# Performance work log

Hardware: AMD Instinct MI355X
Metric: run time of the kernel (lower is better)

The kernel has to match this reference:

```python
import jax, jax.numpy as jnp
import numpy as np

D_MODEL = 1024
HEADS = 16
D_K = D_MODEL // HEADS
B, S = 2, 2048
NEG = -1e9


def setup_inputs() -> dict:
    key = jax.random.key(0)
    ks = jax.random.split(key, 12)
    sc = 1.0 / np.sqrt(D_MODEL)
    inp = {
        'query': jax.random.normal(ks[0], (B, S, D_MODEL), jnp.float32),
        'key': jax.random.normal(ks[1], (B, S, D_MODEL), jnp.float32),
        'value': jax.random.normal(ks[2], (B, S, D_MODEL), jnp.float32),
        'mask': jnp.tril(jnp.ones((S, S), jnp.int32))[None, None],  # [1,1,S,S] causal
        'Wq': jax.random.normal(ks[3], (D_MODEL, D_MODEL), jnp.float32) * sc,
        'bq': jax.random.normal(ks[4], (D_MODEL,), jnp.float32) * 0.02,
        'Wk': jax.random.normal(ks[5], (D_MODEL, D_MODEL), jnp.float32) * sc,
        'bk': jax.random.normal(ks[6], (D_MODEL,), jnp.float32) * 0.02,
        'Wv': jax.random.normal(ks[7], (D_MODEL, D_MODEL), jnp.float32) * sc,
        'bv': jax.random.normal(ks[8], (D_MODEL,), jnp.float32) * 0.02,
        'Wo': jax.random.normal(ks[9], (D_MODEL, D_MODEL), jnp.float32) * sc,
        'bo': jax.random.normal(ks[10], (D_MODEL,), jnp.float32) * 0.02,
    }
    return inp


def reference(query, key, value, mask, Wq, bq, Wk, bk, Wv, bv, Wo, bo):
    # QKV projections (torch Linear: x @ W.T + b; here W stored as [in,out])
    def split_heads(x):  # [B,S,D] -> [B,H,S,dk]
        return x.reshape(B, S, HEADS, D_K).transpose(0, 2, 1, 3)

    q = split_heads(query @ Wq + bq)
    k = split_heads(key @ Wk + bk)
    v = split_heads(value @ Wv + bv)

    scores = jnp.einsum('bhqd,bhkd->bhqk', q, k) / np.sqrt(D_K)
    scores = jnp.where(mask == 0, NEG, scores)
    attn = jax.nn.softmax(scores, axis=-1)  # dropout p=0 (eval) -> identity
    out = jnp.einsum('bhqk,bhkd->bhqd', attn, v)
    out = out.transpose(0, 2, 1, 3).reshape(B, S, D_MODEL)
    return out @ Wo + bo
```

## Files before the change

### kernel.cpp

```cpp
#include <hip/hip_runtime.h>
#include <hip/hip_bf16.h>
#include <cstdint>
#include <cstddef>

typedef short short8 __attribute__((ext_vector_type(8)));
typedef float f32x4 __attribute__((ext_vector_type(4)));
typedef float f32x16 __attribute__((ext_vector_type(16)));

#define SS 2048
#define DK 64
#define LAMBDA 0.18033688011112042f

__device__ __forceinline__ float b2f(ushort u) {
    union { uint32_t i; float f; } x; x.i = ((uint32_t)u) << 16; return x.f;
}
__device__ __forceinline__ ushort f2b(float f) {
    union { float f; uint32_t i; } x; x.f = f;
    uint32_t r = (x.i + 0x7fffu + ((x.i >> 16) & 1u)) >> 16;
    return (ushort)r;
}
__device__ __forceinline__ uint32_t pk_bf16(float a, float b) {
    union { __hip_bfloat162 v; uint32_t u; } x;
    float2 f2; f2.x = a; f2.y = b;
    x.v = __float22bfloat162_rn(f2);
    return x.u;
}

__device__ __forceinline__ void gl_lds16(const ushort* __restrict__ g, ushort* l) {
    __builtin_amdgcn_global_load_lds(
        (const __attribute__((address_space(1))) uint32_t*)(uintptr_t)g,
        (__attribute__((address_space(3))) uint32_t*)(uintptr_t)l, 16, 0, 0);
}

__device__ __forceinline__ bool probe_bf16(const uint32_t* __restrict__ probe) {
    const int lane = threadIdx.x & 63;
    int c = 0;
#pragma unroll
    for (int i = 0; i < 4; ++i) {
        uint32_t u = probe[lane * 4 + i];
        uint32_t e = (u >> 7) & 0xffu;
        c += (e >= 100u && e <= 140u) ? 1 : 0;
    }
    unsigned long long b = __ballot(c >= 3);
    return __popcll(b) > 32;
}

__device__ __forceinline__ void ld8_f32_to_bf16(ushort* dst, const float* __restrict__ src) {
    float4 a = *(const float4*)src;
    float4 b = *(const float4*)(src + 4);
    ushort t[8] = {f2b(a.x), f2b(a.y), f2b(a.z), f2b(a.w),
                   f2b(b.x), f2b(b.y), f2b(b.z), f2b(b.w)};
    *(uint4*)dst = *(uint4*)t;
}

__global__ __launch_bounds__(256) void transpose_all(const void* __restrict__ W0,
                                                     const void* __restrict__ W1,
                                                     const void* __restrict__ W2,
                                                     const void* __restrict__ W3,
                                                     ushort* __restrict__ ws,
                                                     const uint32_t* __restrict__ probe,
                                                     size_t wotOff) {
    __shared__ __align__(16) ushort t[64 * 72];
    const bool isbf = probe_bf16(probe);
    const int z = blockIdx.z;
    const void* W = (z == 0) ? W0 : (z == 1) ? W1 : (z == 2) ? W2 : W3;
    ushort* T = ws + ((z < 3) ? ((size_t)z << 20) : wotOff);

    const int n0 = blockIdx.x * 64, k0 = blockIdx.y * 64;
    const int tid = threadIdx.x;
    const int r = tid >> 3, cg = (tid & 7) * 8;
    if (isbf) {
        const ushort* Wb = (const ushort*)W;
#pragma unroll
        for (int p = 0; p < 2; ++p) {
            int k = r + p * 32;
            *(uint4*)&t[k * 72 + cg] = *(const uint4*)&Wb[(size_t)(k0 + k) * 1024 + n0 + cg];
        }
    } else {
        const float* Wf = (const float*)W;
#pragma unroll
        for (int p = 0; p < 2; ++p) {
            int k = r + p * 32;
            ld8_f32_to_bf16(&t[k * 72 + cg], &Wf[(size_t)(k0 + k) * 1024 + n0 + cg]);
        }
    }
    __syncthreads();
#pragma unroll
    for (int p = 0; p < 2; ++p) {
        int n = r + p * 32;
        uint4 o;
        ushort* op = (ushort*)&o;
#pragma unroll
        for (int i = 0; i < 8; ++i) op[i] = t[(cg + i) * 72 + n];
        *(uint4*)&T[(size_t)(n0 + n) * 1024 + k0 + cg] = o;
    }
}

__global__ __launch_bounds__(256) void conv_qkv(const void* __restrict__ q,
                                                const void* __restrict__ k,
                                                const void* __restrict__ v,
                                                ushort* __restrict__ ws,
                                                const uint32_t* __restrict__ probe,
                                                size_t dstOff) {
    const bool isbf = probe_bf16(probe);
    const int z = blockIdx.y;
    const void* src = (z == 0) ? q : (z == 1) ? k : v;
    ushort* dst = ws + dstOff + ((size_t)z << 22);
    const size_t i = ((size_t)blockIdx.x * 256 + threadIdx.x) * 8;
    if (isbf)
        *(uint4*)&dst[i] = *(const uint4*)&((const ushort*)src)[i];
    else
        ld8_f32_to_bf16(&dst[i], &((const float*)src)[i]);
}

template <int PRE>
__global__ __launch_bounds__(256) void qkv_gemm(const void* __restrict__ qp,
                                                const void* __restrict__ kp,
                                                const void* __restrict__ vp,
                                                const void* __restrict__ bqp,
                                                const void* __restrict__ bkp,
                                                const void* __restrict__ bvp,
                                                ushort* __restrict__ ws,
                                                const uint32_t* __restrict__ probe) {
    __shared__ __align__(16) ushort As[128 * 32];
    __shared__ __align__(16) ushort Bs[128 * 32];
    const bool isbf = probe_bf16(probe);
    const int z = blockIdx.z;
    const ushort* Bt = ws + ((size_t)z << 20);
    const void* bias = (z == 0) ? bqp : (z == 1) ? bkp : bvp;
    ushort* C = ws + ((size_t)((PRE ? 16 : 5) + 4 * z) << 20);
    const float scl = (z == 0) ? LAMBDA : 1.0f;

    const int tid = threadIdx.x;
    const int lane = tid & 63, wid = tid >> 6;
    const int l15 = lane & 15, g = lane >> 4;
    const int wm = wid >> 1, wn = wid & 1;
    const int m0 = blockIdx.y * 128, n0 = blockIdx.x * 128;
    const int sr = tid >> 2, sc = (tid & 3) * 8;
    const int lrow = (lane >> 2), lcol = (lane & 3) * 8;

    f32x4 acc[4][4];
#pragma unroll
    for (int i = 0; i < 4; ++i)
#pragma unroll
        for (int j = 0; j < 4; ++j) {
            f32x4 zz = {0.f, 0.f, 0.f, 0.f};
            acc[i][j] = zz;
        }

    for (int kk = 0; kk < 1024; kk += 32) {
        __syncthreads();
#pragma unroll
        for (int q = 0; q < 2; ++q) {
            const int row = (wid * 2 + q) * 16 + lrow;
            gl_lds16(&Bt[(size_t)(n0 + row) * 1024 + kk + lcol], &Bs[(wid * 2 + q) * 512]);
        }
        if (PRE) {
            const ushort* Ab = ws + ((size_t)(4 + 4 * z) << 20);
#pragma unroll
            for (int q = 0; q < 2; ++q) {
                const int row = (wid * 2 + q) * 16 + lrow;
                gl_lds16(&Ab[(size_t)(m0 + row) * 1024 + kk + lcol], &As[(wid * 2 + q) * 512]);
            }
        } else {
            const void* A = (z == 0) ? qp : (z == 1) ? kp : vp;
            if (isbf) {
                const ushort* Ab = (const ushort*)A;
#pragma unroll
                for (int q = 0; q < 2; ++q) {
                    const int row = (wid * 2 + q) * 16 + lrow;
                    gl_lds16(&Ab[(size_t)(m0 + row) * 1024 + kk + lcol], &As[(wid * 2 + q) * 512]);
                }
            } else {
                const float* Af = (const float*)A;
                ld8_f32_to_bf16(&As[sr * 32 + sc], &Af[(size_t)(m0 + sr) * 1024 + kk + sc]);
                ld8_f32_to_bf16(&As[(sr + 64) * 32 + sc],
                                &Af[(size_t)(m0 + sr + 64) * 1024 + kk + sc]);
            }
        }
        __syncthreads();
        short8 a[4], b[4];
#pragma unroll
        for (int i = 0; i < 4; ++i) a[i] = *(const short8*)&As[(wm * 64 + i * 16 + l15) * 32 + g * 8];
#pragma unroll
        for (int j = 0; j < 4; ++j) b[j] = *(const short8*)&Bs[(wn * 64 + j * 16 + l15) * 32 + g * 8];
#pragma unroll
        for (int i = 0; i < 4; ++i)
#pragma unroll
            for (int j = 0; j < 4; ++j)
                acc[i][j] = __builtin_amdgcn_mfma_f32_16x16x32_bf16(a[i], b[j], acc[i][j], 0, 0, 0);
    }

#pragma unroll
    for (int i = 0; i < 4; ++i)
#pragma unroll
        for (int j = 0; j < 4; ++j) {
            const int col = n0 + wn * 64 + j * 16 + l15;
            const float bv = isbf ? b2f(((const ushort*)bias)[col]) : ((const float*)bias)[col];
#pragma unroll
            for (int r = 0; r < 4; ++r) {
                const int row = m0 + wm * 64 + i * 16 + g * 4 + r;
                const float v = (acc[i][j][r] + bv) * scl;
                size_t idx;
                if (z != 2) {
                    idx = ((size_t)((row >> 11) * 16 + (col >> 6)) * SS + (row & 2047)) * 64 +
                          (col & 63);
                } else {
                    idx = ((size_t)((row >> 11) * 16 + (col >> 6)) * 64 + (col & 63)) * SS +
                          (row & 2047);
                }
                C[idx] = f2b(v);
            }
        }
}

__global__ __launch_bounds__(256) void out_gemm(const ushort* __restrict__ A,
                                                const ushort* __restrict__ Bt,
                                                const void* __restrict__ bias,
                                                void* __restrict__ C,
                                                const uint32_t* __restrict__ probe) {
    __shared__ __align__(16) ushort As[64 * 32];
    __shared__ __align__(16) ushort Bs[128 * 32];
    const bool isbf = probe_bf16(probe);
    const int tid = threadIdx.x;
    const int lane = tid & 63, wid = tid >> 6;
    const int l15 = lane & 15, g = lane >> 4;
    const int wm = wid >> 1, wn = wid & 1;
    const int m0 = blockIdx.y * 64, n0 = blockIdx.x * 128;
    const int lrow = (lane >> 2), lcol = (lane & 3) * 8;

    f32x4 acc[2][4];
#pragma unroll
    for (int i = 0; i < 2; ++i)
#pragma unroll
        for (int j = 0; j < 4; ++j) {
            f32x4 zz = {0.f, 0.f, 0.f, 0.f};
            acc[i][j] = zz;
        }

    for (int kk = 0; kk < 1024; kk += 32) {
        __syncthreads();
        {
            const int row = wid * 16 + lrow;
            gl_lds16(&A[(size_t)(m0 + row) * 1024 + kk + lcol], &As[wid * 512]);
        }
#pragma unroll
        for (int q = 0; q < 2; ++q) {
            const int row = (wid * 2 + q) * 16 + lrow;
            gl_lds16(&Bt[(size_t)(n0 + row) * 1024 + kk + lcol], &Bs[(wid * 2 + q) * 512]);
        }
        __syncthreads();
        short8 a[2], b[4];
#pragma unroll
        for (int i = 0; i < 2; ++i) a[i] = *(const short8*)&As[(wm * 32 + i * 16 + l15) * 32 + g * 8];
#pragma unroll
        for (int j = 0; j < 4; ++j) b[j] = *(const short8*)&Bs[(wn * 64 + j * 16 + l15) * 32 + g * 8];
#pragma unroll
        for (int i = 0; i < 2; ++i)
#pragma unroll
            for (int j = 0; j < 4; ++j)
                acc[i][j] = __builtin_amdgcn_mfma_f32_16x16x32_bf16(a[i], b[j], acc[i][j], 0, 0, 0);
    }

#pragma unroll
    for (int i = 0; i < 2; ++i)
#pragma unroll
        for (int j = 0; j < 4; ++j) {
            const int col = n0 + wn * 64 + j * 16 + l15;
            const float bv = isbf ? b2f(((const ushort*)bias)[col]) : ((const float*)bias)[col];
#pragma unroll
            for (int r = 0; r < 4; ++r) {
                const int row = m0 + wm * 32 + i * 16 + g * 4 + r;
                const float v = acc[i][j][r] + bv;
                const size_t idx = (size_t)row * 1024 + col;
                if (isbf)
                    ((ushort*)C)[idx] = f2b(v);
                else
                    ((float*)C)[idx] = v;
            }
        }
}

__global__ __launch_bounds__(256, 2) void attn_fwd(const ushort* __restrict__ Q,
                                                   const ushort* __restrict__ K,
                                                   const ushort* __restrict__ Vt,
                                                   ushort* __restrict__ O) {
    __shared__ __align__(16) ushort Ks[2][64 * 64];
    __shared__ __align__(16) ushort Vs[2][64 * 64];

    const int y = blockIdx.y;
    const int s0i = (blockIdx.x + y) & 15;
    const int t = (y & 16) ? (15 - s0i) : s0i;
    const int tid = threadIdx.x;
    const int lane = tid & 63, wid = tid >> 6;
    const int l31 = lane & 31, h = lane >> 5;

    const ushort* Qb = Q + (size_t)y * SS * DK;
    const ushort* Kb = K + (size_t)y * SS * DK;
    const ushort* Vb = Vt + (size_t)y * DK * SS;
    const int b = y >> 4, hh = y & 15;

    const int q0w = t * 128 + wid * 32;
    const int nkt = 2 * t + 2;

    const int srow = lane >> 3;
    const int sgc = ((lane & 7) ^ srow) * 8;

    short8 qf[4];
#pragma unroll
    for (int k4 = 0; k4 < 4; ++k4)
        qf[k4] = *(const short8*)&Qb[(size_t)(q0w + l31) * 64 + k4 * 16 + h * 8];

    int foff[2][4];
#pragma unroll
    for (int aa = 0; aa < 2; ++aa)
#pragma unroll
        for (int k4 = 0; k4 < 4; ++k4)
            foff[aa][k4] = (aa * 32 + l31) * 64 + (((k4 * 2 + h) ^ (l31 & 7)) * 8);

    f32x16 acc[2];
#pragma unroll
    for (int nt = 0; nt < 2; ++nt)
#pragma unroll
        for (int r = 0; r < 16; ++r) acc[nt][r] = 0.f;
    float lpA = 0.f, lpB = 0.f;

#pragma unroll
    for (int i = 0; i < 2; ++i) {
        const int chunk = wid * 2 + i;
        const int row = chunk * 8 + srow;
        gl_lds16(&Kb[(size_t)row * 64 + sgc], &Ks[0][chunk * 512]);
        gl_lds16(&Vb[(size_t)row * SS + sgc], &Vs[0][chunk * 512]);
    }
    __syncthreads();

#pragma unroll 1
    for (int kt = 0; kt < nkt; ++kt) {
        const int cur = kt & 1;
        if (kt + 1 < nkt) {
            const int k0n = (kt + 1) * 64;
#pragma unroll
            for (int i = 0; i < 2; ++i) {
                const int chunk = wid * 2 + i;
                const int row = chunk * 8 + srow;
                gl_lds16(&Kb[(size_t)(k0n + row) * 64 + sgc], &Ks[cur ^ 1][chunk * 512]);
                gl_lds16(&Vb[(size_t)row * SS + k0n + sgc], &Vs[cur ^ 1][chunk * 512]);
            }
        }

        if (q0w + 31 >= kt * 64) {
            f32x16 sc[2];
#pragma unroll
            for (int st = 0; st < 2; ++st)
#pragma unroll
                for (int r = 0; r < 16; ++r) sc[st][r] = 0.f;
#pragma unroll
            for (int st = 0; st < 2; ++st)
#pragma unroll
                for (int k4 = 0; k4 < 4; ++k4) {
                    short8 kb = *(const short8*)&Ks[cur][foff[st][k4]];
                    sc[st] = __builtin_amdgcn_mfma_f32_32x32x16_bf16(kb, qf[k4], sc[st], 0, 0, 0);
                }

            if (kt >= nkt - 2) {
                const int qg = q0w + l31;
#pragma unroll
                for (int st = 0; st < 2; ++st)
#pragma unroll
                    for (int r = 0; r < 16; ++r) {
                        const int kvg = kt * 64 + st * 32 + (r & 3) + 8 * (r >> 2) + 4 * h;
                        if (kvg > qg) sc[st][r] = -1e9f;
                    }
            }

            uint32_t pk8[2][8];
#pragma unroll
            for (int st = 0; st < 2; ++st) {
                float ls = 0.f;
#pragma unroll
                for (int i = 0; i < 8; ++i) {
                    const float p0 = exp2f(sc[st][2 * i]);
                    const float p1 = exp2f(sc[st][2 * i + 1]);
                    ls += p0 + p1;
                    pk8[st][i] = pk_bf16(p0, p1);
                }
                if (st == 0) lpA += ls; else lpB += ls;
            }

#pragma unroll
            for (int st = 0; st < 2; ++st) {
                asm("v_permlane32_swap_b32 %0, %1" : "+v"(pk8[st][0]), "+v"(pk8[st][2]));
                asm("v_permlane32_swap_b32 %0, %1" : "+v"(pk8[st][1]), "+v"(pk8[st][3]));
                asm("v_permlane32_swap_b32 %0, %1" : "+v"(pk8[st][4]), "+v"(pk8[st][6]));
                asm("v_permlane32_swap_b32 %0, %1" : "+v"(pk8[st][5]), "+v"(pk8[st][7]));
            }

#pragma unroll
            for (int ktv = 0; ktv < 4; ++ktv) {
                union { uint32_t u[4]; short8 s; } pa;
#pragma unroll
                for (int w4 = 0; w4 < 4; ++w4) pa.u[w4] = pk8[ktv >> 1][(ktv & 1) * 4 + w4];
#pragma unroll
                for (int nt = 0; nt < 2; ++nt) {
                    short8 vb = *(const short8*)&Vs[cur][foff[nt][ktv]];
                    acc[nt] =
                        __builtin_amdgcn_mfma_f32_32x32x16_bf16(pa.s, vb, acc[nt], 0, 0, 0);
                }
            }
        }

        __syncthreads();
    }

    const float lp = lpA + lpB;
    const float lt = lp + __shfl_xor(lp, 32);
    const float inv = 1.0f / lt;
#pragma unroll
    for (int r = 0; r < 16; ++r) {
        const int qrow = (r & 3) + 8 * (r >> 2) + 4 * h;
        const float ivr = __shfl(inv, qrow);
        const int rowg = q0w + qrow;
#pragma unroll
        for (int nt = 0; nt < 2; ++nt) {
            const int col = hh * 64 + nt * 32 + l31;
            O[(size_t)(b * SS + rowg) * 1024 + col] = f2b(acc[nt][r] * ivr);
        }
    }
}

extern "C" void kernel_launch(void* const* d_in, const int* in_sizes, int n_in,
                              void* d_out, int out_size, void* d_ws, size_t ws_size,
                              hipStream_t stream) {
    const void* q = d_in[0];
    const void* k = d_in[1];
    const void* v = d_in[2];
    const void* Wq = d_in[4];
    const void* bq = d_in[5];
    const void* Wk = d_in[6];
    const void* bk = d_in[7];
    const void* Wv = d_in[8];
    const void* bv = d_in[9];
    const void* Wo = d_in[10];
    const void* bo = d_in[11];
    const uint32_t* probe = (const uint32_t*)d_in[0];

    ushort* ws = (ushort*)d_ws;
    const size_t M = (size_t)1 << 20;
    const bool pre = ws_size >= 28 * M * sizeof(ushort);

    if (pre) {
        transpose_all<<<dim3(16, 16, 4), 256, 0, stream>>>(Wq, Wk, Wv, Wo, ws, probe, 3 * M);
        conv_qkv<<<dim3(2048, 3), 256, 0, stream>>>(q, k, v, ws, probe, 4 * M);
        qkv_gemm<1><<<dim3(8, 32, 3), 256, 0, stream>>>(q, k, v, bq, bk, bv, ws, probe);
        attn_fwd<<<dim3(16, 32), 256, 0, stream>>>(ws + 16 * M, ws + 20 * M, ws + 24 * M,
                                                   ws + 4 * M);
        out_gemm<<<dim3(8, 64), 256, 0, stream>>>(ws + 4 * M, ws + 3 * M, bo, d_out, probe);
    } else {
        transpose_all<<<dim3(16, 16, 4), 256, 0, stream>>>(Wq, Wk, Wv, Wo, ws, probe, 4 * M);
        qkv_gemm<0><<<dim3(8, 32, 3), 256, 0, stream>>>(q, k, v, bq, bk, bv, ws, probe);
        attn_fwd<<<dim3(16, 32), 256, 0, stream>>>(ws + 5 * M, ws + 9 * M, ws + 13 * M, ws);
        out_gemm<<<dim3(8, 64), 256, 0, stream>>>(ws, ws + 4 * M, bo, d_out, probe);
    }
}
```

Measured before the change: 237.8 us.

## Double-buffer LDS tiles and swizzle block order in QKV and output GEMMs

Both projection GEMMs now keep two LDS buffers, so the next K-slice is loaded while MFMAs run on the current one, with a single barrier per iteration instead of two. The block index is also remapped so that consecutive blocks share the same N tile column, which should improve L2 reuse of the weight tiles. LDS use per block doubles, which could lower occupancy. The swizzle hard-codes grid dimensions (8 columns, 32 or 64 row tiles).

```diff
diff --git a/kernel.cpp b/kernel.cpp
--- a/kernel.cpp
+++ b/kernel.cpp
@@ -122,8 +122,8 @@
                                                 const void* __restrict__ bvp,
                                                 ushort* __restrict__ ws,
                                                 const uint32_t* __restrict__ probe) {
-    __shared__ __align__(16) ushort As[128 * 32];
-    __shared__ __align__(16) ushort Bs[128 * 32];
+    __shared__ __align__(16) ushort As[2][128 * 32];
+    __shared__ __align__(16) ushort Bs[2][128 * 32];
     const bool isbf = probe_bf16(probe);
     const int z = blockIdx.z;
     const ushort* Bt = ws + ((size_t)z << 20);
@@ -135,7 +135,9 @@
     const int lane = tid & 63, wid = tid >> 6;
     const int l15 = lane & 15, g = lane >> 4;
     const int wm = wid >> 1, wn = wid & 1;
-    const int m0 = blockIdx.y * 128, n0 = blockIdx.x * 128;
+    const int id0 = blockIdx.y * 8 + blockIdx.x;
+    const int id = (id0 & 7) * 32 + (id0 >> 3);
+    const int m0 = (id >> 3) * 128, n0 = (id & 7) * 128;
     const int sr = tid >> 2, sc = (tid & 3) * 8;
     const int lrow = (lane >> 2), lcol = (lane & 3) * 8;
 
@@ -148,19 +150,19 @@
             acc[i][j] = zz;
         }
 
-    for (int kk = 0; kk < 1024; kk += 32) {
-        __syncthreads();
+    auto stageAB = [&](int kk, int bsel) {
 #pragma unroll
         for (int q = 0; q < 2; ++q) {
             const int row = (wid * 2 + q) * 16 + lrow;
-            gl_lds16(&Bt[(size_t)(n0 + row) * 1024 + kk + lcol], &Bs[(wid * 2 + q) * 512]);
+            gl_lds16(&Bt[(size_t)(n0 + row) * 1024 + kk + lcol], &Bs[bsel][(wid * 2 + q) * 512]);
         }
         if (PRE) {
             const ushort* Ab = ws + ((size_t)(4 + 4 * z) << 20);
 #pragma unroll
             for (int q = 0; q < 2; ++q) {
                 const int row = (wid * 2 + q) * 16 + lrow;
-                gl_lds16(&Ab[(size_t)(m0 + row) * 1024 + kk + lcol], &As[(wid * 2 + q) * 512]);
+                gl_lds16(&Ab[(size_t)(m0 + row) * 1024 + kk + lcol],
+                         &As[bsel][(wid * 2 + q) * 512]);
             }
         } else {
             const void* A = (z == 0) ? qp : (z == 1) ? kp : vp;
@@ -169,26 +171,37 @@
 #pragma unroll
                 for (int q = 0; q < 2; ++q) {
                     const int row = (wid * 2 + q) * 16 + lrow;
-                    gl_lds16(&Ab[(size_t)(m0 + row) * 1024 + kk + lcol], &As[(wid * 2 + q) * 512]);
+                    gl_lds16(&Ab[(size_t)(m0 + row) * 1024 + kk + lcol],
+                             &As[bsel][(wid * 2 + q) * 512]);
                 }
             } else {
                 const float* Af = (const float*)A;
-                ld8_f32_to_bf16(&As[sr * 32 + sc], &Af[(size_t)(m0 + sr) * 1024 + kk + sc]);
-                ld8_f32_to_bf16(&As[(sr + 64) * 32 + sc],
+                ld8_f32_to_bf16(&As[bsel][sr * 32 + sc], &Af[(size_t)(m0 + sr) * 1024 + kk + sc]);
+                ld8_f32_to_bf16(&As[bsel][(sr + 64) * 32 + sc],
                                 &Af[(size_t)(m0 + sr + 64) * 1024 + kk + sc]);
             }
         }
-        __syncthreads();
+    };
+
+    stageAB(0, 0);
+    __syncthreads();
+#pragma unroll 2
+    for (int kk = 0; kk < 1024; kk += 32) {
+        const int cur = (kk >> 5) & 1;
+        if (kk < 1024 - 32) stageAB(kk + 32, cur ^ 1);
         short8 a[4], b[4];
 #pragma unroll
-        for (int i = 0; i < 4; ++i) a[i] = *(const short8*)&As[(wm * 64 + i * 16 + l15) * 32 + g * 8];
-#pragma unroll
-        for (int j = 0; j < 4; ++j) b[j] = *(const short8*)&Bs[(wn * 64 + j * 16 + l15) * 32 + g * 8];
+        for (int i = 0; i < 4; ++i)
+            a[i] = *(const short8*)&As[cur][(wm * 64 + i * 16 + l15) * 32 + g * 8];
+#pragma unroll
+        for (int j = 0; j < 4; ++j)
+            b[j] = *(const short8*)&Bs[cur][(wn * 64 + j * 16 + l15) * 32 + g * 8];
 #pragma unroll
         for (int i = 0; i < 4; ++i)
 #pragma unroll
             for (int j = 0; j < 4; ++j)
                 acc[i][j] = __builtin_amdgcn_mfma_f32_16x16x32_bf16(a[i], b[j], acc[i][j], 0, 0, 0);
+        __syncthreads();
     }
 
 #pragma unroll
@@ -219,14 +232,16 @@
                                                 const void* __restrict__ bias,
                                                 void* __restrict__ C,
                                                 const uint32_t* __restrict__ probe) {
-    __shared__ __align__(16) ushort As[64 * 32];
-    __shared__ __align__(16) ushort Bs[128 * 32];
+    __shared__ __align__(16) ushort As[2][64 * 32];
+    __shared__ __align__(16) ushort Bs[2][128 * 32];
     const bool isbf = probe_bf16(probe);
     const int tid = threadIdx.x;
     const int lane = tid & 63, wid = tid >> 6;
     const int l15 = lane & 15, g = lane >> 4;
     const int wm = wid >> 1, wn = wid & 1;
-    const int m0 = blockIdx.y * 64, n0 = blockIdx.x * 128;
+    const int id0 = blockIdx.y * 8 + blockIdx.x;
+    const int id = (id0 & 7) * 64 + (id0 >> 3);
+    const int m0 = (id >> 3) * 64, n0 = (id & 7) * 128;
     const int lrow = (lane >> 2), lcol = (lane & 3) * 8;
 
     f32x4 acc[2][4];
@@ -238,28 +253,37 @@
             acc[i][j] = zz;
         }
 
-    for (int kk = 0; kk < 1024; kk += 32) {
-        __syncthreads();
+    auto stageAB = [&](int kk, int bsel) {
         {
             const int row = wid * 16 + lrow;
-            gl_lds16(&A[(size_t)(m0 + row) * 1024 + kk + lcol], &As[wid * 512]);
+            gl_lds16(&A[(size_t)(m0 + row) * 1024 + kk + lcol], &As[bsel][wid * 512]);
         }
 #pragma unroll
         for (int q = 0; q < 2; ++q) {
             const int row = (wid * 2 + q) * 16 + lrow;
-            gl_lds16(&Bt[(size_t)(n0 + row) * 1024 + kk + lcol], &Bs[(wid * 2 + q) * 512]);
-        }
-        __syncthreads();
+            gl_lds16(&Bt[(size_t)(n0 + row) * 1024 + kk + lcol], &Bs[bsel][(wid * 2 + q) * 512]);
+        }
+    };
+
+    stageAB(0, 0);
+    __syncthreads();
+#pragma unroll 2
+    for (int kk = 0; kk < 1024; kk += 32) {
+        const int cur = (kk >> 5) & 1;
+        if (kk < 1024 - 32) stageAB(kk + 32, cur ^ 1);
         short8 a[2], b[4];
 #pragma unroll
-        for (int i = 0; i < 2; ++i) a[i] = *(const short8*)&As[(wm * 32 + i * 16 + l15) * 32 + g * 8];
-#pragma unroll
-        for (int j = 0; j < 4; ++j) b[j] = *(const short8*)&Bs[(wn * 64 + j * 16 + l15) * 32 + g * 8];
+        for (int i = 0; i < 2; ++i)
+            a[i] = *(const short8*)&As[cur][(wm * 32 + i * 16 + l15) * 32 + g * 8];
+#pragma unroll
+        for (int j = 0; j < 4; ++j)
+            b[j] = *(const short8*)&Bs[cur][(wn * 64 + j * 16 + l15) * 32 + g * 8];
 #pragma unroll
         for (int i = 0; i < 2; ++i)
 #pragma unroll
             for (int j = 0; j < 4; ++j)
                 acc[i][j] = __builtin_amdgcn_mfma_f32_16x16x32_bf16(a[i], b[j], acc[i][j], 0, 0, 0);
+        __syncthreads();
     }
 
 #pragma unroll
```

After: 230.4 us. 3.1% less time.
